# Performance work log

Measured on AMD Instinct MI355X. Metric: run time of the kernel, lower is better.

Reference implementation:

```python
import jax, jax.numpy as jnp
import numpy as np

N, D = 8192, 128


def setup_inputs() -> dict:
    key = jax.random.key(0)
    k1, k2 = jax.random.split(key)
    z1 = jax.random.normal(k1, (N, D), dtype=jnp.float32)
    z2 = jax.random.normal(k2, (N, D), dtype=jnp.float32)
    return {"z1": z1, "z2": z2}


def reference(z1, z2):
    # logits[i, j] = -||z1_i - z2_j||^2, computed via the cdist-as-GEMM identity
    # (same math as dz = z2[None,:,:] - z1[:,None,:]; -einsum('...d,...d->...', dz, dz))
    sq1 = jnp.sum(z1 * z1, axis=-1)  # [N]
    sq2 = jnp.sum(z2 * z2, axis=-1)  # [N]
    logits = 2.0 * (z1 @ z2.T) - sq1[:, None] - sq2[None, :]  # [N, N]
    # CrossEntropyLoss with labels = arange(N): mean over rows of -log_softmax diag
    logp = jax.nn.log_softmax(logits, axis=-1)
    return -jnp.mean(jnp.diagonal(logp))
```

## Files before the change

kernel.cpp:

```cpp
#include <hip/hip_runtime.h>
#include <hip/hip_bf16.h>

typedef unsigned int   u32;
typedef unsigned short u16;

#define NN   8192
#define DD   128
#define CCH  16
#define CHUNK (NN / CCH)
#define JT   64
#define LDST 136

#define LOG2E 1.4426950408889634f
#define LN2F  0.6931471805599453f
#define BIAS  32.0f

typedef __bf16 bf16x8 __attribute__((ext_vector_type(8)));
typedef float  f32x4  __attribute__((ext_vector_type(4)));

__device__ __forceinline__ u16 f2bf(float x) {
    u32 u = __float_as_uint(x);
    u += 0x7fffu + ((u >> 16) & 1u);
    return (u16)(u >> 16);
}

__global__ __launch_bounds__(256) void prep_kernel(
    const float* __restrict__ z1, const float* __restrict__ z2,
    u32* __restrict__ b1, u32* __restrict__ b2,
    float* __restrict__ negsq2b, float* __restrict__ diag)
{
    int row  = blockIdx.x * 4 + (threadIdx.x >> 6);
    int lane = threadIdx.x & 63;
    float2 a = reinterpret_cast<const float2*>(z1)[row * 64 + lane];
    float2 b = reinterpret_cast<const float2*>(z2)[row * 64 + lane];
    b1[row * 64 + lane] = (u32)f2bf(a.x) | ((u32)f2bf(a.y) << 16);
    b2[row * 64 + lane] = (u32)f2bf(b.x) | ((u32)f2bf(b.y) << 16);
    float dot = a.x * b.x + a.y * b.y;
    float sq  = b.x * b.x + b.y * b.y;
    #pragma unroll
    for (int o = 32; o > 0; o >>= 1) {
        dot += __shfl_xor(dot, o);
        sq  += __shfl_xor(sq, o);
    }
    if (lane == 0) {
        negsq2b[row] = -sq * LOG2E - BIAS;
        diag[row]    = 2.0f * dot - sq;
    }
}

__global__ __launch_bounds__(256, 4) void score_kernel(
    const u16* __restrict__ b1, const u16* __restrict__ b2,
    const float* __restrict__ negsq2b, float* __restrict__ partS)
{
    __shared__ alignas(16) u16 tile[JT * LDST];
    const int tid  = threadIdx.x;
    const int lane = tid & 63;
    const int wid  = tid >> 6;
    const int llo  = lane & 15, lhi = lane >> 4;
    const int chunk = blockIdx.x;
    const int i0    = blockIdx.y * 128 + wid * 32;
    const int j0    = chunk * CHUNK;

    bf16x8 zf0[4], zf1[4];
    #pragma unroll
    for (int kk = 0; kk < 4; ++kk) {
        zf0[kk] = *reinterpret_cast<const bf16x8*>(b1 + (size_t)(i0 + llo)      * DD + kk * 32 + lhi * 8);
        zf1[kk] = *reinterpret_cast<const bf16x8*>(b1 + (size_t)(i0 + 16 + llo) * DD + kk * 32 + lhi * 8);
    }

    float sum0 = 0.f, sum1 = 0.f;
    const float C2 = 2.0f * LOG2E;

    for (int jt = 0; jt < CHUNK; jt += JT) {
        __syncthreads();
        #pragma unroll
        for (int u = 0; u < 4; ++u) {
            int idx = u * 256 + tid;
            int row = idx >> 4, colb = idx & 15;
            *reinterpret_cast<uint4*>(&tile[row * LDST + colb * 8]) =
                *reinterpret_cast<const uint4*>(b2 + (size_t)(j0 + jt + row) * DD + colb * 8);
        }
        __syncthreads();
        #pragma unroll
        for (int jj = 0; jj < 4; ++jj) {
            bf16x8 av[4];
            const int ar = jj * 16 + llo;
            #pragma unroll
            for (int kk = 0; kk < 4; ++kk)
                av[kk] = *reinterpret_cast<const bf16x8*>(&tile[ar * LDST + kk * 32 + lhi * 8]);
            f32x4 acc0 = {0.f, 0.f, 0.f, 0.f};
            f32x4 acc1 = {0.f, 0.f, 0.f, 0.f};
            #pragma unroll
            for (int kk = 0; kk < 4; ++kk) {
                acc0 = __builtin_amdgcn_mfma_f32_16x16x32_bf16(av[kk], zf0[kk], acc0, 0, 0, 0);
                acc1 = __builtin_amdgcn_mfma_f32_16x16x32_bf16(av[kk], zf1[kk], acc1, 0, 0, 0);
            }
            const float4 nsq = *reinterpret_cast<const float4*>(negsq2b + j0 + jt + jj * 16 + lhi * 4);
            const float nq[4] = {nsq.x, nsq.y, nsq.z, nsq.w};
            #pragma unroll
            for (int r = 0; r < 4; ++r) {
                sum0 += __builtin_amdgcn_exp2f(fmaf(acc0[r], C2, nq[r]));
                sum1 += __builtin_amdgcn_exp2f(fmaf(acc1[r], C2, nq[r]));
            }
        }
    }
    sum0 += __shfl_xor(sum0, 16); sum0 += __shfl_xor(sum0, 32);
    sum1 += __shfl_xor(sum1, 16); sum1 += __shfl_xor(sum1, 32);
    if (lhi == 0) {
        partS[(size_t)chunk * NN + i0 + llo]      = sum0;
        partS[(size_t)chunk * NN + i0 + 16 + llo] = sum1;
    }
}

__global__ __launch_bounds__(256) void finalize1_kernel(
    const float* __restrict__ partS, const float* __restrict__ diag,
    float* __restrict__ blocksum)
{
    __shared__ float red[4];
    int r = blockIdx.x * 256 + threadIdx.x;
    float s = 0.f;
    #pragma unroll
    for (int c = 0; c < CCH; ++c) s += partS[(size_t)c * NN + r];
    float lse = (BIAS + __builtin_amdgcn_logf(s)) * LN2F;
    float acc = lse - diag[r];
    #pragma unroll
    for (int o = 32; o > 0; o >>= 1) acc += __shfl_xor(acc, o);
    int lane = threadIdx.x & 63, wid = threadIdx.x >> 6;
    if (lane == 0) red[wid] = acc;
    __syncthreads();
    if (threadIdx.x == 0)
        blocksum[blockIdx.x] = red[0] + red[1] + red[2] + red[3];
}

__global__ void finalize2_kernel(const float* __restrict__ blocksum, float* __restrict__ out)
{
    int lane = threadIdx.x;
    float v = (lane < 32) ? blocksum[lane] : 0.f;
    #pragma unroll
    for (int o = 32; o > 0; o >>= 1) v += __shfl_xor(v, o);
    if (lane == 0) out[0] = v * (1.0f / (float)NN);
}

extern "C" void kernel_launch(void* const* d_in, const int* in_sizes, int n_in,
                              void* d_out, int out_size, void* d_ws, size_t ws_size,
                              hipStream_t stream)
{
    const float* z1 = (const float*)d_in[0];
    const float* z2 = (const float*)d_in[1];
    char* ws = (char*)d_ws;

    const size_t bf_bytes = (size_t)NN * DD * 2;
    u32*   b1       = (u32*)ws;
    u32*   b2       = (u32*)(ws + bf_bytes);
    float* negsq2b  = (float*)(ws + 2 * bf_bytes);
    float* diag     = (float*)(ws + 2 * bf_bytes + (size_t)NN * 4);
    float* partS    = (float*)(ws + 2 * bf_bytes + (size_t)NN * 8);
    float* blocksum = (float*)(ws + 2 * bf_bytes + (size_t)NN * 8 + (size_t)CCH * NN * 4);
    float* out      = (float*)d_out;

    prep_kernel<<<NN / 4, 256, 0, stream>>>(z1, z2, b1, b2, negsq2b, diag);
    score_kernel<<<dim3(CCH, NN / 128), 256, 0, stream>>>((const u16*)b1, (const u16*)b2, negsq2b, partS);
    finalize1_kernel<<<NN / 256, 256, 0, stream>>>(partS, diag, blocksum);
    finalize2_kernel<<<1, 64, 0, stream>>>(blocksum, out);
}
```

Baseline: 37.21 us.

## Use 32x32 MFMA tiles with double-buffered direct-to-LDS loads and XOR swizzle

The score kernel now uses 32x32x16 bf16 MFMAs. Each wave covers 64 query rows instead of 32, which halves the number of blocks along i and doubles reuse of each staged z2 tile. Staging goes through global_load_lds into a double-buffered shared tile with an XOR swizzle in place of padding, so the next tile's load overlaps compute and LDS bank conflicts are avoided. The exp epilogue uses packed float2 FMAs and four partial accumulators. The cost is higher register pressure (occupancy hint lowered to 2) and fewer blocks overall.

```diff
diff --git a/kernel.cpp b/kernel.cpp
--- a/kernel.cpp
+++ b/kernel.cpp
@@ -9,14 +9,15 @@
 #define CCH  16
 #define CHUNK (NN / CCH)
 #define JT   64
-#define LDST 136
+#define NT   (CHUNK / JT)
 
 #define LOG2E 1.4426950408889634f
 #define LN2F  0.6931471805599453f
 #define BIAS  32.0f
 
 typedef __bf16 bf16x8 __attribute__((ext_vector_type(8)));
-typedef float  f32x4  __attribute__((ext_vector_type(4)));
+typedef float  f32x16 __attribute__((ext_vector_type(16)));
+typedef float  f32x2  __attribute__((ext_vector_type(2)));
 
 __device__ __forceinline__ u16 f2bf(float x) {
     u32 u = __float_as_uint(x);
@@ -48,67 +49,97 @@
     }
 }
 
-__global__ __launch_bounds__(256, 4) void score_kernel(
+__global__ __launch_bounds__(256, 2) void score_kernel(
     const u16* __restrict__ b1, const u16* __restrict__ b2,
     const float* __restrict__ negsq2b, float* __restrict__ partS)
 {
-    __shared__ alignas(16) u16 tile[JT * LDST];
+    __shared__ alignas(16) u16 tile[2][JT * DD];
     const int tid  = threadIdx.x;
     const int lane = tid & 63;
     const int wid  = tid >> 6;
-    const int llo  = lane & 15, lhi = lane >> 4;
+    const int r    = lane & 31, hi = lane >> 5;
     const int chunk = blockIdx.x;
-    const int i0    = blockIdx.y * 128 + wid * 32;
     const int j0    = chunk * CHUNK;
+    const int i0w   = blockIdx.y * 256 + wid * 64;
 
-    bf16x8 zf0[4], zf1[4];
+    bf16x8 zf0[8], zf1[8];
     #pragma unroll
-    for (int kk = 0; kk < 4; ++kk) {
-        zf0[kk] = *reinterpret_cast<const bf16x8*>(b1 + (size_t)(i0 + llo)      * DD + kk * 32 + lhi * 8);
-        zf1[kk] = *reinterpret_cast<const bf16x8*>(b1 + (size_t)(i0 + 16 + llo) * DD + kk * 32 + lhi * 8);
+    for (int kk = 0; kk < 8; ++kk) {
+        zf0[kk] = *reinterpret_cast<const bf16x8*>(b1 + (size_t)(i0w + r)      * DD + kk * 16 + hi * 8);
+        zf1[kk] = *reinterpret_cast<const bf16x8*>(b1 + (size_t)(i0w + 32 + r) * DD + kk * 16 + hi * 8);
     }
 
-    float sum0 = 0.f, sum1 = 0.f;
-    const float C2 = 2.0f * LOG2E;
+    const int sl   = lane & 15;
+    const int rrow = lane >> 4;
 
-    for (int jt = 0; jt < CHUNK; jt += JT) {
-        __syncthreads();
+    auto stage = [&](int t, int buf) {
         #pragma unroll
         for (int u = 0; u < 4; ++u) {
-            int idx = u * 256 + tid;
-            int row = idx >> 4, colb = idx & 15;
-            *reinterpret_cast<uint4*>(&tile[row * LDST + colb * 8]) =
-                *reinterpret_cast<const uint4*>(b2 + (size_t)(j0 + jt + row) * DD + colb * 8);
+            int row   = wid * 16 + u * 4 + rrow;
+            int gslot = sl ^ (row & 15);
+            const u16* src = b2 + (size_t)(j0 + t * JT + row) * DD + gslot * 8;
+            u16* dst = &tile[buf][(wid * 16 + u * 4) * DD];
+            __builtin_amdgcn_global_load_lds(
+                (const __attribute__((address_space(1))) void*)src,
+                (__attribute__((address_space(3))) void*)dst, 16, 0, 0);
         }
+    };
+
+    float s0 = 0.f, s1 = 0.f, s2 = 0.f, s3 = 0.f;
+    const f32x2 C2v = {2.0f * LOG2E, 2.0f * LOG2E};
+    const int sw = r & 15;
+
+    int cur = 0;
+    stage(0, 0);
+    for (int t = 0; t < NT; ++t) {
         __syncthreads();
+        if (t + 1 < NT) stage(t + 1, cur ^ 1);
+        const u16* tp = tile[cur];
         #pragma unroll
-        for (int jj = 0; jj < 4; ++jj) {
-            bf16x8 av[4];
-            const int ar = jj * 16 + llo;
+        for (int jj = 0; jj < 2; ++jj) {
+            const float* nqb = negsq2b + j0 + t * JT + jj * 32 + 4 * hi;
+            float4 nq0 = *reinterpret_cast<const float4*>(nqb);
+            float4 nq1 = *reinterpret_cast<const float4*>(nqb + 8);
+            float4 nq2 = *reinterpret_cast<const float4*>(nqb + 16);
+            float4 nq3 = *reinterpret_cast<const float4*>(nqb + 24);
+            bf16x8 av[8];
             #pragma unroll
-            for (int kk = 0; kk < 4; ++kk)
-                av[kk] = *reinterpret_cast<const bf16x8*>(&tile[ar * LDST + kk * 32 + lhi * 8]);
-            f32x4 acc0 = {0.f, 0.f, 0.f, 0.f};
-            f32x4 acc1 = {0.f, 0.f, 0.f, 0.f};
+            for (int kk = 0; kk < 8; ++kk) {
+                int off = (jj * 32 + r) * DD + (((2 * kk + hi) ^ sw) << 3);
+                av[kk] = *reinterpret_cast<const bf16x8*>(tp + off);
+            }
+            f32x16 acc0 = {0.f}; f32x16 acc1 = {0.f};
             #pragma unroll
-            for (int kk = 0; kk < 4; ++kk) {
-                acc0 = __builtin_amdgcn_mfma_f32_16x16x32_bf16(av[kk], zf0[kk], acc0, 0, 0, 0);
-                acc1 = __builtin_amdgcn_mfma_f32_16x16x32_bf16(av[kk], zf1[kk], acc1, 0, 0, 0);
+            for (int kk = 0; kk < 8; ++kk) {
+                acc0 = __builtin_amdgcn_mfma_f32_32x32x16_bf16(av[kk], zf0[kk], acc0, 0, 0, 0);
+                acc1 = __builtin_amdgcn_mfma_f32_32x32x16_bf16(av[kk], zf1[kk], acc1, 0, 0, 0);
             }
-            const float4 nsq = *reinterpret_cast<const float4*>(negsq2b + j0 + jt + jj * 16 + lhi * 4);
-            const float nq[4] = {nsq.x, nsq.y, nsq.z, nsq.w};
+            const float nqa[16] = {nq0.x, nq0.y, nq0.z, nq0.w,
+                                   nq1.x, nq1.y, nq1.z, nq1.w,
+                                   nq2.x, nq2.y, nq2.z, nq2.w,
+                                   nq3.x, nq3.y, nq3.z, nq3.w};
             #pragma unroll
-            for (int r = 0; r < 4; ++r) {
-                sum0 += __builtin_amdgcn_exp2f(fmaf(acc0[r], C2, nq[r]));
-                sum1 += __builtin_amdgcn_exp2f(fmaf(acc1[r], C2, nq[r]));
+            for (int q = 0; q < 8; ++q) {
+                f32x2 n2 = {nqa[2 * q], nqa[2 * q + 1]};
+                f32x2 a0 = {acc0[2 * q], acc0[2 * q + 1]};
+                f32x2 t0 = a0 * C2v + n2;
+                s0 += __builtin_amdgcn_exp2f(t0.x);
+                s1 += __builtin_amdgcn_exp2f(t0.y);
+                f32x2 a1 = {acc1[2 * q], acc1[2 * q + 1]};
+                f32x2 t1 = a1 * C2v + n2;
+                s2 += __builtin_amdgcn_exp2f(t1.x);
+                s3 += __builtin_amdgcn_exp2f(t1.y);
             }
         }
+        cur ^= 1;
     }
-    sum0 += __shfl_xor(sum0, 16); sum0 += __shfl_xor(sum0, 32);
-    sum1 += __shfl_xor(sum1, 16); sum1 += __shfl_xor(sum1, 32);
-    if (lhi == 0) {
-        partS[(size_t)chunk * NN + i0 + llo]      = sum0;
-        partS[(size_t)chunk * NN + i0 + 16 + llo] = sum1;
+
+    float sum0 = s0 + s1, sum1 = s2 + s3;
+    sum0 += __shfl_xor(sum0, 32);
+    sum1 += __shfl_xor(sum1, 32);
+    if (hi == 0) {
+        partS[(size_t)chunk * NN + i0w + r]      = sum0;
+        partS[(size_t)chunk * NN + i0w + 32 + r] = sum1;
     }
 }
 
@@ -159,7 +190,7 @@
     float* out      = (float*)d_out;
 
     prep_kernel<<<NN / 4, 256, 0, stream>>>(z1, z2, b1, b2, negsq2b, diag);
-    score_kernel<<<dim3(CCH, NN / 128), 256, 0, stream>>>((const u16*)b1, (const u16*)b2, negsq2b, partS);
+    score_kernel<<<dim3(CCH, NN / 256), 256, 0, stream>>>((const u16*)b1, (const u16*)b2, negsq2b, partS);
     finalize1_kernel<<<NN / 256, 256, 0, stream>>>(partS, diag, blocksum);
     finalize2_kernel<<<1, 64, 0, stream>>>(blocksum, out);
 }
```

After: 35.96 us. -3.4%, faster.
